# Kernel tuning notes

Hardware: AMD Instinct MI355X
Metric: run time of the kernel (lower is better)

## Reference

```python
import jax, jax.numpy as jnp
import numpy as np

NE, NR = 100000, 200
STT, ABS, REL, RDIM = 512, 256, 256, 384
GAMMA = 12.0
PI = 3.141592653589793
EMB_RNG_R = float(np.sqrt(6.0 / (NR + RDIM)))
B = 8192


def setup_inputs() -> dict:
    key = jax.random.key(0)
    ks = jax.random.split(key, 16)
    cols = [
        jax.random.randint(ks[0], (B, 1), 0, NE),      # s
        jax.random.randint(ks[1], (B, 1), 0, NR),      # r
        jax.random.randint(ks[2], (B, 1), 0, NE),      # o
        jax.random.randint(ks[3], (B, 1), 0, 31),      # d
        jax.random.randint(ks[4], (B, 1), 0, 12),      # m
        jax.random.randint(ks[5], (B, 1), 0, 100),     # y
        jax.random.randint(ks[6], (B, 2 * NR), 0, 1000),  # context times
    ]
    x = jnp.concatenate(cols, axis=1).astype(jnp.int64)
    s = 0.02
    return {
        "x": x,
        "e_emb": jax.random.normal(ks[7], (NE, STT), jnp.float32) * s,
        "r_emb": jax.random.normal(ks[8], (NR, RDIM), jnp.float32) * s,
        "d_frq": jax.random.normal(ks[9], (NE, ABS), jnp.float32) * s,
        "d_phi": jax.random.normal(ks[10], (NE, ABS), jnp.float32) * s,
        "d_amp": jax.random.normal(ks[11], (NE, ABS // 2), jnp.float32) * s,
        "m_frq": jax.random.normal(ks[12], (NE, ABS), jnp.float32) * s,
        "m_phi": jax.random.normal(ks[13], (NE, ABS), jnp.float32) * s,
        "m_amp": jax.random.normal(ks[14], (NE, ABS // 2), jnp.float32) * s,
        "w_e": jax.random.normal(ks[15], (STT, REL // 2), jnp.float32) * s,
        "w_rp": jax.random.normal(jax.random.fold_in(key, 99), (NR, NR, 1), jnp.float32) * s,
    }


def _pos_emb(t):  # t: float [N] -> [N, REL]
    f = 1.0 / (10000.0 ** (jnp.arange(0, REL, 2, dtype=jnp.float32) / REL))
    rs = t[:, None] * f[None, :]
    return jnp.concatenate([jnp.cos(rs), jnp.sin(rs)], axis=1)


def reference(x, e_emb, r_emb, d_frq, d_phi, d_amp, m_frq, m_phi, m_amp, w_e, w_rp):
    f32 = jnp.float32

    def t_emb(e, d, m):  # e int [B], d,m float [B,1] -> [B, ABS]
        re_d, im_d = jnp.split(d * d_frq[e] + d_phi[e], 2, axis=1)
        ad = d_amp[e]
        demb = jnp.concatenate([ad * jnp.cos(re_d), ad * jnp.sin(im_d)], axis=1)
        re_m, im_m = jnp.split(m * m_frq[e] + m_phi[e], 2, axis=1)
        am = m_amp[e]
        memb = jnp.concatenate([am * jnp.cos(re_m), am * jnp.sin(im_m)], axis=1)
        return demb + memb

    def e_p_emb(e):  # e: [B,1,STT] -> [B,1,REL]
        re_w, im_w = jnp.split(w_e, 2, axis=0)
        re_e, im_e = jnp.split(e, 2, axis=2)
        re_p = re_e @ re_w - im_e @ im_w
        im_p = im_e @ re_w - re_e @ im_w  # note: minus, matching source
        return jnp.concatenate([re_p, im_p], axis=2)

    def e_r_emb(r_idx, e_t):  # e_t: [B,NR] float -> [B,REL,1]
        er = _pos_emb(e_t.reshape(-1)).reshape(e_t.shape[0], NR, REL)
        er = jnp.transpose(er, (0, 2, 1))  # [B,REL,NR]
        return jnp.einsum('bdn,bno->bdo', er, w_rp[r_idx])

    s_idx, r_idx, o_idx = x[:, 0], x[:, 1], x[:, 2]
    d_abs = x[:, 3:4].astype(f32)
    m_abs = x[:, 4:5].astype(f32)
    c_s = x[:, -2 * NR:-NR].astype(f32)
    c_o = x[:, -NR:].astype(f32)

    s = e_emb[s_idx][:, None, :]
    s_t = t_emb(s_idx, d_abs, m_abs)[:, None, :]
    s_p = e_p_emb(s)
    s_r = e_r_emb(r_idx, c_s)

    o = e_emb[o_idx][:, None, :]
    o_t = t_emb(o_idx, d_abs, m_abs)[:, None, :]
    o_p = e_p_emb(o)
    o_r = e_r_emb(r_idx, c_o)

    r = r_emb[r_idx][:, None, :]  # [B,1,RDIM]
    p_r = r / (EMB_RNG_R / PI)
    re_r, im_r = jnp.cos(p_r), jnp.sin(p_r)

    re_s, im_s = jnp.split(s, 2, axis=2)
    re_st, im_st = jnp.split(s_t, 2, axis=2)
    re_s = jnp.concatenate([re_s, re_st], axis=2)  # [B,1,RDIM]
    im_s = jnp.concatenate([im_s, im_st], axis=2)
    re_o, im_o = jnp.split(o, 2, axis=2)
    re_ot, im_ot = jnp.split(o_t, 2, axis=2)
    re_o = jnp.concatenate([re_o, re_ot], axis=2)
    im_o = jnp.concatenate([im_o, im_ot], axis=2)

    # RotatE complex rotation score on static+absolute part
    re_sc = re_s * re_r - im_s * im_r - re_o
    im_sc = re_s * im_r + im_s * re_r - im_o
    sc_abs = jnp.sqrt(re_sc * re_sc + im_sc * im_sc).sum(axis=2)

    # relative-time score from projected embeddings + relation-context embeddings
    s_rel = s_p + jnp.transpose(s_r, (0, 2, 1))  # [B,1,REL]
    o_rel = o_p + jnp.transpose(o_r, (0, 2, 1))
    re_sr, im_sr = jnp.split(s_rel, 2, axis=2)
    re_or, im_or = jnp.split(o_rel, 2, axis=2)
    dre, dim = re_sr - re_or, im_sr - im_or
    sc_rel = jnp.sqrt(dre * dre + dim * dim).sum(axis=2)

    return GAMMA - (sc_abs + sc_rel)  # [B,1]
```

## Files before the change

### kernel.cpp

```cpp
#include <hip/hip_runtime.h>
#include <cstdint>

#define B_ROWS 8192
#define XSTR   406
#define GAMMA_C 12.0f
#define SCALE_ANG 30.994217f

#define KH     1024

#define NG_BLK 2048
#define NS_BLK 4096
#define NT_BLK 128
#define NW_BLK 64
#define NPREP  (NG_BLK + NS_BLK + NT_BLK + NW_BLK)

#define TF_BYTES    (KH*256*2)
#define WCAT_BYTES  (512*256*2)
#define G_BYTES     (8192*KH*2)
#define SAB_BYTES   (8192*4)
#define WS_FULL     ((size_t)(TF_BYTES + WCAT_BYTES + G_BYTES + SAB_BYTES))
#define OLDTAB_BYTES (1000*256*2)
#define WS_OLD       ((size_t)(OLDTAB_BYTES + WCAT_BYTES))

typedef __attribute__((ext_vector_type(8))) short short8v;
typedef __attribute__((ext_vector_type(4))) float float4v;

__device__ __forceinline__ float bfLo(uint32_t u) { return __uint_as_float(u << 16); }
__device__ __forceinline__ float bfHi(uint32_t u) { return __uint_as_float(u & 0xffff0000u); }
__device__ __forceinline__ float bf1(unsigned short u) { return __uint_as_float((uint32_t)u << 16); }

__device__ __forceinline__ uint32_t f2bf_u(float x) {
  uint32_t u = __float_as_uint(x);
  u += 0x7fffu + ((u >> 16) & 1u);
  return u >> 16;
}
__device__ __forceinline__ unsigned short f2bf(float x) { return (unsigned short)f2bf_u(x); }

__device__ __forceinline__ short8v cvt8(float4 a, float4 b) {
  short8v r;
  r[0] = (short)f2bf(a.x); r[1] = (short)f2bf(a.y);
  r[2] = (short)f2bf(a.z); r[3] = (short)f2bf(a.w);
  r[4] = (short)f2bf(b.x); r[5] = (short)f2bf(b.y);
  r[6] = (short)f2bf(b.z); r[7] = (short)f2bf(b.w);
  return r;
}

__global__ __launch_bounds__(256) void kge_prep2(
    const int* __restrict__ x, const float* __restrict__ w_rp,
    const float* __restrict__ w_e, const float* __restrict__ e_emb,
    const float* __restrict__ r_emb,
    const float* __restrict__ d_frq, const float* __restrict__ d_phi, const float* __restrict__ d_amp,
    const float* __restrict__ m_frq, const float* __restrict__ m_phi, const float* __restrict__ m_amp,
    unsigned short* __restrict__ tf, unsigned short* __restrict__ wcat,
    unsigned short* __restrict__ G, float* __restrict__ sabs_buf) {
  __shared__ float Hl[4][KH];
  __shared__ float st2[2][2][256];
  __shared__ float redl[4];
  const int bid = blockIdx.x;
  const int tid = threadIdx.x;
  const int sub = tid >> 6, l = tid & 63;

  if (bid < NG_BLK) {
    const int row = bid * 4 + sub;
    float4 z = {0, 0, 0, 0};
    for (int i = l; i < KH / 4; i += 64) ((float4*)Hl[sub])[i] = z;
    const int rid = x[(size_t)row * XSTR + 1];
    const int* cp = x + (size_t)row * XSTR + 6;
    const float* wp = w_rp + (size_t)rid * 200;
    for (int n = l; n < 200; n += 64) {
      float wv = wp[n];
      atomicAdd(&Hl[sub][cp[n]], wv);
      atomicAdd(&Hl[sub][cp[200 + n]], -wv);
    }
    unsigned short* dst = G + (size_t)row * KH;
    for (int i = l; i < KH / 2; i += 64) {
      float a = Hl[sub][2 * i], b = Hl[sub][2 * i + 1];
      ((uint32_t*)dst)[i] = f2bf_u(a) | (f2bf_u(b) << 16);
    }
  } else if (bid < NG_BLK + NS_BLK) {
    const int rsub = tid >> 7;
    const int row = (bid - NG_BLK) * 2 + rsub;
    const int j = tid & 127;
    const int* xr = x + (size_t)row * XSTR;
    const int eS = xr[0], rid = xr[1], eO = xr[2];
    const float dv = (float)xr[3], mv = (float)xr[4];
    const int j2 = 2 * j;
    #pragma unroll
    for (int ent = 0; ent < 2; ++ent) {
      const int e = ent ? eO : eS;
      float2 fd = *(const float2*)&d_frq[(size_t)e * 256 + j2];
      float2 pd = *(const float2*)&d_phi[(size_t)e * 256 + j2];
      float2 fm = *(const float2*)&m_frq[(size_t)e * 256 + j2];
      float2 pm = *(const float2*)&m_phi[(size_t)e * 256 + j2];
      const int ja = j2 & 127;
      float2 ad = *(const float2*)&d_amp[(size_t)e * 128 + ja];
      float2 am = *(const float2*)&m_amp[(size_t)e * 128 + ja];
      float a0 = fmaf(dv, fd.x, pd.x), a1 = fmaf(dv, fd.y, pd.y);
      float b0 = fmaf(mv, fm.x, pm.x), b1 = fmaf(mv, fm.y, pm.y);
      float t0, t1, u0, u1;
      if (j2 < 128) { t0 = __cosf(a0); t1 = __cosf(a1); u0 = __cosf(b0); u1 = __cosf(b1); }
      else          { t0 = __sinf(a0); t1 = __sinf(a1); u0 = __sinf(b0); u1 = __sinf(b1); }
      st2[rsub][ent][j2]     = fmaf(ad.x, t0, am.x * u0);
      st2[rsub][ent][j2 + 1] = fmaf(ad.y, t1, am.y * u1);
    }
    __syncthreads();
    const float* Es = e_emb + (size_t)eS * 512;
    const float* Eo = e_emb + (size_t)eO * 512;
    const float* Rr = r_emb + (size_t)rid * 384;
    float sabs = 0.f;
    #pragma unroll
    for (int t3 = 0; t3 < 3; ++t3) {
      const int u = t3 * 128 + j;
      float ang = Rr[u] * SCALE_ANG;
      float sr = __sinf(ang), cr = __cosf(ang);
      float res, ims, reo, imo;
      if (t3 < 2) {
        res = Es[u]; ims = Es[256 + u];
        reo = Eo[u]; imo = Eo[256 + u];
      } else {
        res = st2[rsub][0][j]; ims = st2[rsub][0][128 + j];
        reo = st2[rsub][1][j]; imo = st2[rsub][1][128 + j];
      }
      float rsc = res * cr - ims * sr - reo;
      float isc = res * sr + ims * cr - imo;
      sabs += sqrtf(rsc * rsc + isc * isc);
    }
    #pragma unroll
    for (int off = 32; off > 0; off >>= 1) sabs += __shfl_down(sabs, off);
    if (l == 0) redl[sub] = sabs;
    __syncthreads();
    if (j == 0) sabs_buf[row] = redl[2 * rsub] + redl[2 * rsub + 1];
  } else if (bid < NG_BLK + NS_BLK + NT_BLK) {
    const int fragid = (bid - NG_BLK - NS_BLK) * 4 + sub;
    const int kt = fragid >> 4, nt = fragid & 15;
    const int c = nt * 16 + (l & 15);
    const float f = exp2f(-(float)(c & 127) * (13.287712379549449f / 128.f));
    __align__(16) unsigned short v[8];
    #pragma unroll
    for (int jj = 0; jj < 8; ++jj) {
      int k = kt * 32 + ((l >> 4) << 3) + jj;
      float val = 0.f;
      if (k < 1000) {
        float s, cv;
        sincosf((float)k * f, &s, &cv);
        val = (c < 128) ? cv : s;
      }
      v[jj] = f2bf(val);
    }
    ((uint4*)tf)[fragid * 64 + l] = *(const uint4*)v;
  } else {
    const int fragid = (bid - NG_BLK - NS_BLK - NT_BLK) * 4 + sub;
    const int kk = fragid >> 4, nt = fragid & 15;
    const int c = nt * 16 + (l & 15);
    __align__(16) unsigned short v[8];
    #pragma unroll
    for (int jj = 0; jj < 8; ++jj) {
      int k = kk * 32 + ((l >> 4) << 3) + jj;
      float s = (k < 256) ? 1.f : -1.f;
      float val = (c < 128) ? s * w_e[k * 128 + c]
                            : -s * w_e[(k ^ 256) * 128 + (c - 128)];
      v[jj] = f2bf(val);
    }
    ((uint4*)wcat)[fragid * 64 + l] = *(const uint4*)v;
  }
}

__global__ __launch_bounds__(256) void kge_fused4(
    const int* __restrict__ x, const float* __restrict__ e_emb,
    const unsigned short* __restrict__ G,
    const unsigned short* __restrict__ wcat, const unsigned short* __restrict__ tf,
    const float* __restrict__ sabs_buf, float* __restrict__ out) {
  __shared__ float part[4][16][256];
  __shared__ float prel[4][16];
  const int tid = threadIdx.x;
  const int w = tid >> 6, l = tid & 63;
  const int m0 = blockIdx.x * 16;

  const int rowA = m0 + (l & 15);
  const int* xrA = x + (size_t)rowA * XSTR;
  const float* Esp = e_emb + (size_t)xrA[0] * 512 + ((l >> 4) << 3);
  const float* Eop = e_emb + (size_t)xrA[2] * 512 + ((l >> 4) << 3);
  const unsigned short* Gp = G + (size_t)rowA * KH + ((l >> 4) << 3);
  const short8v* wq = (const short8v*)wcat;
  const short8v* tq = (const short8v*)tf;

  float4v acc[16];
  #pragma unroll
  for (int i = 0; i < 16; ++i) acc[i] = (float4v){0, 0, 0, 0};

  const int k0 = w * 12;
  #pragma unroll 2
  for (int kt = k0; kt < k0 + 12; ++kt) {
    short8v a;
    const short8v* bsrc;
    if (kt < 16) {
      float4 s0 = *(const float4*)(Esp + kt * 32);
      float4 s1 = *(const float4*)(Esp + kt * 32 + 4);
      float4 o0 = *(const float4*)(Eop + kt * 32);
      float4 o1 = *(const float4*)(Eop + kt * 32 + 4);
      float4 d0 = {s0.x - o0.x, s0.y - o0.y, s0.z - o0.z, s0.w - o0.w};
      float4 d1 = {s1.x - o1.x, s1.y - o1.y, s1.z - o1.z, s1.w - o1.w};
      a = cvt8(d0, d1);
      bsrc = wq + (size_t)kt * 1024;
    } else {
      a = *(const short8v*)(Gp + (kt - 16) * 32);
      bsrc = tq + (size_t)(kt - 16) * 1024;
    }
    #pragma unroll
    for (int nt = 0; nt < 16; ++nt)
      acc[nt] = __builtin_amdgcn_mfma_f32_16x16x32_bf16(a, bsrc[nt * 64 + l], acc[nt], 0, 0, 0);
  }
  #pragma unroll
  for (int nt = 0; nt < 16; ++nt)
    #pragma unroll
    for (int q = 0; q < 4; ++q)
      part[w][nt][q * 64 + l] = acc[nt][q];
  __syncthreads();

  {
    float sq[4] = {0.f, 0.f, 0.f, 0.f};
    #pragma unroll
    for (int pp = 0; pp < 2; ++pp) {
      const int p = 2 * w + pp;
      #pragma unroll
      for (int q = 0; q < 4; ++q) {
        float dre = part[0][p][q * 64 + l] + part[1][p][q * 64 + l]
                  + part[2][p][q * 64 + l] + part[3][p][q * 64 + l];
        float dim = part[0][p + 8][q * 64 + l] + part[1][p + 8][q * 64 + l]
                  + part[2][p + 8][q * 64 + l] + part[3][p + 8][q * 64 + l];
        sq[q] += sqrtf(dre * dre + dim * dim);
      }
    }
    #pragma unroll
    for (int q = 0; q < 4; ++q) {
      float s = sq[q];
      s += __shfl_xor(s, 1); s += __shfl_xor(s, 2);
      s += __shfl_xor(s, 4); s += __shfl_xor(s, 8);
      if ((l & 15) == 0) prel[w][(l >> 4) * 4 + q] = s;
    }
  }
  __syncthreads();
  if (tid < 16) {
    const int r = tid;
    float srel = prel[0][r] + prel[1][r] + prel[2][r] + prel[3][r];
    out[m0 + r] = GAMMA_C - (sabs_buf[m0 + r] + srel);
  }
}

#define NTH    512
#define RPB    8
#define ERB    (2*RPB)
#define APAD   520

__global__ void kge_table_old(unsigned short* __restrict__ tab) {
  int t = blockIdx.x;
  int j = threadIdx.x;
  double f = pow(10000.0, -(double)j / 128.0);
  double ang = (double)t * f;
  int q = j >> 1, lo = j & 1;
  tab[t * 256 + 4 * q + lo]     = f2bf((float)cos(ang));
  tab[t * 256 + 4 * q + 2 + lo] = f2bf((float)sin(ang));
}

__global__ void kge_wcat_old(const float* __restrict__ w_e, unsigned short* __restrict__ wcat) {
  int bid = blockIdx.x;
  int kk = bid >> 4, nt = bid & 15;
  int l = threadIdx.x;
  __align__(16) unsigned short v[8];
  int c = nt * 16 + (l & 15);
  #pragma unroll
  for (int j = 0; j < 8; ++j) {
    int k = kk * 32 + ((l >> 4) << 3) + j;
    float s = (k < 256) ? 1.f : -1.f;
    float val = (c < 128) ? s * w_e[k * 128 + c]
                          : -s * w_e[(k ^ 256) * 128 + (c - 128)];
    v[j] = f2bf(val);
  }
  ((uint4*)wcat)[bid * 64 + l] = *(const uint4*)v;
}

__global__ __launch_bounds__(NTH, 4) void kge_main3(
    const int* __restrict__ x,
    const float* __restrict__ e_emb, const float* __restrict__ r_emb,
    const float* __restrict__ d_frq, const float* __restrict__ d_phi, const float* __restrict__ d_amp,
    const float* __restrict__ m_frq, const float* __restrict__ m_phi, const float* __restrict__ m_amp,
    const float* __restrict__ w_rp,
    const unsigned short* __restrict__ tab, const unsigned short* __restrict__ wcat,
    float* __restrict__ out) {
  __shared__ __align__(16) unsigned short A[ERB][APAD];
  __shared__ __align__(16) unsigned short stb[ERB][256];
  __shared__ __align__(16) float p[ERB][256];
  __shared__ int meta[RPB][6];

  const int tid = threadIdx.x;
  const int base_row = blockIdx.x * RPB;
  const int w = tid >> 6, l = tid & 63;

  if (tid < RPB * 6) {
    int r = tid / 6, f = tid % 6;
    meta[r][f] = x[(size_t)(base_row + r) * XSTR + f];
  }
  __syncthreads();

  for (int i = tid; i < ERB * 128; i += NTH) {
    int er = i >> 7, k4 = i & 127;
    int e = (er & 1) ? meta[er >> 1][2] : meta[er >> 1][0];
    float4 v = ((const float4*)e_emb)[(size_t)e * 128 + k4];
    uint2 pk;
    pk.x = f2bf_u(v.x) | (f2bf_u(v.y) << 16);
    pk.y = f2bf_u(v.z) | (f2bf_u(v.w) << 16);
    *(uint2*)&A[er][k4 * 4] = pk;
  }
  for (int it = tid; it < ERB * 256; it += NTH) {
    int j = it & 255, er = it >> 8, r = er >> 1;
    int e = (er & 1) ? meta[r][2] : meta[r][0];
    float dv = (float)meta[r][3], mv = (float)meta[r][4];
    size_t b256 = (size_t)e * 256 + j, b128 = (size_t)e * 128 + (j & 127);
    float argd = fmaf(dv, d_frq[b256], d_phi[b256]);
    float argm = fmaf(mv, m_frq[b256], m_phi[b256]);
    float vd = (j < 128) ? d_amp[b128] * __cosf(argd) : d_amp[b128] * __sinf(argd);
    float vm = (j < 128) ? m_amp[b128] * __cosf(argm) : m_amp[b128] * __sinf(argm);
    stb[er][j] = f2bf(vd + vm);
  }

  float s0 = 0, s1 = 0, s2 = 0, s3 = 0, o0 = 0, o1 = 0, o2 = 0, o3 = 0;
  {
    const int wu  = __builtin_amdgcn_readfirstlane(w);
    const int rid = __builtin_amdgcn_readfirstlane(meta[wu][1]);
    const int*   cp = x + (size_t)(base_row + wu) * XSTR + 6;
    const float* wp = w_rp + (size_t)rid * 200;
    const uint2* tl = ((const uint2*)tab) + l;
    #pragma unroll 2
    for (int n = 0; n < 200; ++n) {
      float wv = wp[n];
      int cS = cp[n];
      int cO = cp[200 + n];
      uint2 qs = tl[(size_t)cS * 64];
      uint2 qo = tl[(size_t)cO * 64];
      s0 = fmaf(wv, bfLo(qs.x), s0); s1 = fmaf(wv, bfHi(qs.x), s1);
      s2 = fmaf(wv, bfLo(qs.y), s2); s3 = fmaf(wv, bfHi(qs.y), s3);
      o0 = fmaf(wv, bfLo(qo.x), o0); o1 = fmaf(wv, bfHi(qo.x), o1);
      o2 = fmaf(wv, bfLo(qo.y), o2); o3 = fmaf(wv, bfHi(qo.y), o3);
    }
  }
  __syncthreads();

  {
    float4v acc0 = {0, 0, 0, 0}, acc1 = {0, 0, 0, 0};
    const int nt0 = 2 * w, nt1 = 2 * w + 1;
    const short8v* bp = (const short8v*)wcat;
    const unsigned short* arow = &A[l & 15][(l >> 4) << 3];
    #pragma unroll 8
    for (int kk = 0; kk < 16; ++kk) {
      short8v a  = *(const short8v*)(arow + kk * 32);
      short8v b0 = bp[(kk * 16 + nt0) * 64 + l];
      short8v b1 = bp[(kk * 16 + nt1) * 64 + l];
      acc0 = __builtin_amdgcn_mfma_f32_16x16x32_bf16(a, b0, acc0, 0, 0, 0);
      acc1 = __builtin_amdgcn_mfma_f32_16x16x32_bf16(a, b1, acc1, 0, 0, 0);
    }
    int col = l & 15, rbase = (l >> 4) * 4;
    #pragma unroll
    for (int q = 0; q < 4; ++q) {
      p[rbase + q][nt0 * 16 + col] = acc0[q];
      p[rbase + q][nt1 * 16 + col] = acc1[q];
    }
  }
  __syncthreads();

  {
    int es = 2 * w, eo = 2 * w + 1;
    p[es][2 * l] += s0; p[es][2 * l + 1] += s1;
    p[es][128 + 2 * l] += s2; p[es][129 + 2 * l] += s3;
    p[eo][2 * l] += o0; p[eo][2 * l + 1] += o1;
    p[eo][128 + 2 * l] += o2; p[eo][129 + 2 * l] += o3;
  }
  __syncthreads();

  {
    int r = w;
    int rid = meta[r][1];
    float sabs = 0.f;
    #pragma unroll
    for (int u0 = 0; u0 < 384; u0 += 64) {
      int u = u0 + l;
      float ang = r_emb[(size_t)rid * 384 + u] * SCALE_ANG;
      float sr = __sinf(ang), cr = __cosf(ang);
      float res, ims, reo, imo;
      if (u < 256) {
        res = bf1(A[2 * r][u]);       ims = bf1(A[2 * r][256 + u]);
        reo = bf1(A[2 * r + 1][u]);   imo = bf1(A[2 * r + 1][256 + u]);
      } else {
        int uu = u - 256;
        res = bf1(stb[2 * r][uu]);     ims = bf1(stb[2 * r][128 + uu]);
        reo = bf1(stb[2 * r + 1][uu]); imo = bf1(stb[2 * r + 1][128 + uu]);
      }
      float rsc = res * cr - ims * sr - reo;
      float isc = res * sr + ims * cr - imo;
      sabs += sqrtf(rsc * rsc + isc * isc);
    }
    float srel = 0.f;
    #pragma unroll
    for (int u0 = 0; u0 < 128; u0 += 64) {
      int u = u0 + l;
      float dre = p[2 * r][u] - p[2 * r + 1][u];
      float dim = p[2 * r][128 + u] - p[2 * r + 1][128 + u];
      srel += sqrtf(dre * dre + dim * dim);
    }
    float tot = sabs + srel;
    #pragma unroll
    for (int off = 32; off > 0; off >>= 1) tot += __shfl_down(tot, off);
    if (l == 0) out[base_row + r] = GAMMA_C - tot;
  }
}

extern "C" void kernel_launch(void* const* d_in, const int* in_sizes, int n_in,
                              void* d_out, int out_size, void* d_ws, size_t ws_size,
                              hipStream_t stream) {
  (void)in_sizes; (void)n_in; (void)out_size;
  const int*   x     = (const int*)d_in[0];
  const float* e_emb = (const float*)d_in[1];
  const float* r_emb = (const float*)d_in[2];
  const float* d_frq = (const float*)d_in[3];
  const float* d_phi = (const float*)d_in[4];
  const float* d_amp = (const float*)d_in[5];
  const float* m_frq = (const float*)d_in[6];
  const float* m_phi = (const float*)d_in[7];
  const float* m_amp = (const float*)d_in[8];
  const float* w_e   = (const float*)d_in[9];
  const float* w_rp  = (const float*)d_in[10];
  float* out = (float*)d_out;

  if (ws_size >= WS_FULL) {
    char* base = (char*)d_ws;
    unsigned short* tf    = (unsigned short*)base;
    unsigned short* wcat  = (unsigned short*)(base + TF_BYTES);
    unsigned short* G     = (unsigned short*)(base + TF_BYTES + WCAT_BYTES);
    float*          sabsb = (float*)(base + TF_BYTES + WCAT_BYTES + G_BYTES);
    kge_prep2<<<dim3(NPREP), dim3(256), 0, stream>>>(
        x, w_rp, w_e, e_emb, r_emb, d_frq, d_phi, d_amp, m_frq, m_phi, m_amp,
        tf, wcat, G, sabsb);
    kge_fused4<<<dim3(B_ROWS / 16), dim3(256), 0, stream>>>(
        x, e_emb, G, wcat, tf, sabsb, out);
  } else if (ws_size >= WS_OLD) {
    unsigned short* tab  = (unsigned short*)d_ws;
    unsigned short* wcat = (unsigned short*)((char*)d_ws + OLDTAB_BYTES);
    kge_table_old<<<dim3(1000), dim3(128), 0, stream>>>(tab);
    kge_wcat_old<<<dim3(256), dim3(64), 0, stream>>>(w_e, wcat);
    kge_main3<<<dim3(B_ROWS / RPB), dim3(NTH), 0, stream>>>(
        x, e_emb, r_emb, d_frq, d_phi, d_amp, m_frq, m_phi, m_amp, w_rp,
        tab, wcat, out);
  }
}
```

Measured before the change: 66.82 us.

## Build relation-context histogram in LDS inside fused kernel instead of global G

The per-row scatter histogram of relation-context weights is now built with LDS atomics inside the main MFMA kernel rather than in the prep kernel. This removes the 16 MB bf16 G buffer, which was previously written to global memory and read back. The fused kernel now zeroes a padded 16x1028 LDS tile, scatters into it, and feeds the tile to the MFMAs. The same LDS is reused for the partial-sum reduction. This adds barriers and LDS atomic work to the main kernel, and the larger LDS footprint may lower occupancy.

```diff
diff --git a/kernel.cpp b/kernel.cpp
--- a/kernel.cpp
+++ b/kernel.cpp
@@ -7,18 +7,17 @@
 #define SCALE_ANG 30.994217f
 
 #define KH     1024
-
-#define NG_BLK 2048
+#define HPAD   1028
+
 #define NS_BLK 4096
 #define NT_BLK 128
 #define NW_BLK 64
-#define NPREP  (NG_BLK + NS_BLK + NT_BLK + NW_BLK)
+#define NPREP  (NS_BLK + NT_BLK + NW_BLK)
 
 #define TF_BYTES    (KH*256*2)
 #define WCAT_BYTES  (512*256*2)
-#define G_BYTES     (8192*KH*2)
 #define SAB_BYTES   (8192*4)
-#define WS_FULL     ((size_t)(TF_BYTES + WCAT_BYTES + G_BYTES + SAB_BYTES))
+#define WS_FULL     ((size_t)(TF_BYTES + WCAT_BYTES + SAB_BYTES))
 #define OLDTAB_BYTES (1000*256*2)
 #define WS_OLD       ((size_t)(OLDTAB_BYTES + WCAT_BYTES))
 
@@ -45,41 +44,23 @@
   return r;
 }
 
-__global__ __launch_bounds__(256) void kge_prep2(
-    const int* __restrict__ x, const float* __restrict__ w_rp,
+__global__ __launch_bounds__(256) void kge_prep3(
+    const int* __restrict__ x,
     const float* __restrict__ w_e, const float* __restrict__ e_emb,
     const float* __restrict__ r_emb,
     const float* __restrict__ d_frq, const float* __restrict__ d_phi, const float* __restrict__ d_amp,
     const float* __restrict__ m_frq, const float* __restrict__ m_phi, const float* __restrict__ m_amp,
     unsigned short* __restrict__ tf, unsigned short* __restrict__ wcat,
-    unsigned short* __restrict__ G, float* __restrict__ sabs_buf) {
-  __shared__ float Hl[4][KH];
+    float* __restrict__ sabs_buf) {
   __shared__ float st2[2][2][256];
   __shared__ float redl[4];
   const int bid = blockIdx.x;
   const int tid = threadIdx.x;
   const int sub = tid >> 6, l = tid & 63;
 
-  if (bid < NG_BLK) {
-    const int row = bid * 4 + sub;
-    float4 z = {0, 0, 0, 0};
-    for (int i = l; i < KH / 4; i += 64) ((float4*)Hl[sub])[i] = z;
-    const int rid = x[(size_t)row * XSTR + 1];
-    const int* cp = x + (size_t)row * XSTR + 6;
-    const float* wp = w_rp + (size_t)rid * 200;
-    for (int n = l; n < 200; n += 64) {
-      float wv = wp[n];
-      atomicAdd(&Hl[sub][cp[n]], wv);
-      atomicAdd(&Hl[sub][cp[200 + n]], -wv);
-    }
-    unsigned short* dst = G + (size_t)row * KH;
-    for (int i = l; i < KH / 2; i += 64) {
-      float a = Hl[sub][2 * i], b = Hl[sub][2 * i + 1];
-      ((uint32_t*)dst)[i] = f2bf_u(a) | (f2bf_u(b) << 16);
-    }
-  } else if (bid < NG_BLK + NS_BLK) {
+  if (bid < NS_BLK) {
     const int rsub = tid >> 7;
-    const int row = (bid - NG_BLK) * 2 + rsub;
+    const int row = bid * 2 + rsub;
     const int j = tid & 127;
     const int* xr = x + (size_t)row * XSTR;
     const int eS = xr[0], rid = xr[1], eO = xr[2];
@@ -130,8 +111,8 @@
     if (l == 0) redl[sub] = sabs;
     __syncthreads();
     if (j == 0) sabs_buf[row] = redl[2 * rsub] + redl[2 * rsub + 1];
-  } else if (bid < NG_BLK + NS_BLK + NT_BLK) {
-    const int fragid = (bid - NG_BLK - NS_BLK) * 4 + sub;
+  } else if (bid < NS_BLK + NT_BLK) {
+    const int fragid = (bid - NS_BLK) * 4 + sub;
     const int kt = fragid >> 4, nt = fragid & 15;
     const int c = nt * 16 + (l & 15);
     const float f = exp2f(-(float)(c & 127) * (13.287712379549449f / 128.f));
@@ -149,7 +130,7 @@
     }
     ((uint4*)tf)[fragid * 64 + l] = *(const uint4*)v;
   } else {
-    const int fragid = (bid - NG_BLK - NS_BLK - NT_BLK) * 4 + sub;
+    const int fragid = (bid - NS_BLK - NT_BLK) * 4 + sub;
     const int kk = fragid >> 4, nt = fragid & 15;
     const int c = nt * 16 + (l & 15);
     __align__(16) unsigned short v[8];
@@ -165,22 +146,41 @@
   }
 }
 
-__global__ __launch_bounds__(256) void kge_fused4(
+__global__ __launch_bounds__(256) void kge_fused5(
     const int* __restrict__ x, const float* __restrict__ e_emb,
-    const unsigned short* __restrict__ G,
+    const float* __restrict__ w_rp,
     const unsigned short* __restrict__ wcat, const unsigned short* __restrict__ tf,
     const float* __restrict__ sabs_buf, float* __restrict__ out) {
-  __shared__ float part[4][16][256];
+  __shared__ __align__(16) float lds_f[16 * HPAD];
   __shared__ float prel[4][16];
   const int tid = threadIdx.x;
   const int w = tid >> 6, l = tid & 63;
   const int m0 = blockIdx.x * 16;
 
+  #pragma unroll
+  for (int i = tid; i < 16 * HPAD / 4; i += 256)
+    ((float4*)lds_f)[i] = (float4){0, 0, 0, 0};
+  __syncthreads();
+
+  {
+    const int hr = tid >> 4, sub16 = tid & 15;
+    const int row = m0 + hr;
+    const int* xr = x + (size_t)row * XSTR;
+    const int rid = xr[1];
+    const int* cp = xr + 6;
+    const float* wp = w_rp + (size_t)rid * 200;
+    float* hrow = lds_f + hr * HPAD;
+    for (int n = sub16; n < 200; n += 16) {
+      float wv = wp[n];
+      atomicAdd(&hrow[cp[n]], wv);
+      atomicAdd(&hrow[cp[200 + n]], -wv);
+    }
+  }
+
   const int rowA = m0 + (l & 15);
   const int* xrA = x + (size_t)rowA * XSTR;
   const float* Esp = e_emb + (size_t)xrA[0] * 512 + ((l >> 4) << 3);
   const float* Eop = e_emb + (size_t)xrA[2] * 512 + ((l >> 4) << 3);
-  const unsigned short* Gp = G + (size_t)rowA * KH + ((l >> 4) << 3);
   const short8v* wq = (const short8v*)wcat;
   const short8v* tq = (const short8v*)tf;
 
@@ -188,33 +188,43 @@
   #pragma unroll
   for (int i = 0; i < 16; ++i) acc[i] = (float4v){0, 0, 0, 0};
 
-  const int k0 = w * 12;
-  #pragma unroll 2
-  for (int kt = k0; kt < k0 + 12; ++kt) {
-    short8v a;
-    const short8v* bsrc;
-    if (kt < 16) {
-      float4 s0 = *(const float4*)(Esp + kt * 32);
-      float4 s1 = *(const float4*)(Esp + kt * 32 + 4);
-      float4 o0 = *(const float4*)(Eop + kt * 32);
-      float4 o1 = *(const float4*)(Eop + kt * 32 + 4);
-      float4 d0 = {s0.x - o0.x, s0.y - o0.y, s0.z - o0.z, s0.w - o0.w};
-      float4 d1 = {s1.x - o1.x, s1.y - o1.y, s1.z - o1.z, s1.w - o1.w};
-      a = cvt8(d0, d1);
-      bsrc = wq + (size_t)kt * 1024;
-    } else {
-      a = *(const short8v*)(Gp + (kt - 16) * 32);
-      bsrc = tq + (size_t)(kt - 16) * 1024;
-    }
+  #pragma unroll
+  for (int kt = 4 * w; kt < 4 * w + 4; ++kt) {
+    float4 s0 = *(const float4*)(Esp + kt * 32);
+    float4 s1 = *(const float4*)(Esp + kt * 32 + 4);
+    float4 o0 = *(const float4*)(Eop + kt * 32);
+    float4 o1 = *(const float4*)(Eop + kt * 32 + 4);
+    float4 d0 = {s0.x - o0.x, s0.y - o0.y, s0.z - o0.z, s0.w - o0.w};
+    float4 d1 = {s1.x - o1.x, s1.y - o1.y, s1.z - o1.z, s1.w - o1.w};
+    short8v a = cvt8(d0, d1);
+    const short8v* bsrc = wq + (size_t)kt * 1024;
     #pragma unroll
     for (int nt = 0; nt < 16; ++nt)
       acc[nt] = __builtin_amdgcn_mfma_f32_16x16x32_bf16(a, bsrc[nt * 64 + l], acc[nt], 0, 0, 0);
   }
+  __syncthreads();
+
+  {
+    const float* hbase = lds_f + (l & 15) * HPAD + ((l >> 4) << 3);
+    #pragma unroll
+    for (int g = 8 * w; g < 8 * w + 8; ++g) {
+      float4 h0 = *(const float4*)(hbase + g * 32);
+      float4 h1 = *(const float4*)(hbase + g * 32 + 4);
+      short8v a = cvt8(h0, h1);
+      const short8v* bsrc = tq + (size_t)g * 1024;
+      #pragma unroll
+      for (int nt = 0; nt < 16; ++nt)
+        acc[nt] = __builtin_amdgcn_mfma_f32_16x16x32_bf16(a, bsrc[nt * 64 + l], acc[nt], 0, 0, 0);
+    }
+  }
+  __syncthreads();
+
+  float* part = lds_f;
   #pragma unroll
   for (int nt = 0; nt < 16; ++nt)
     #pragma unroll
     for (int q = 0; q < 4; ++q)
-      part[w][nt][q * 64 + l] = acc[nt][q];
+      part[((w * 16 + nt) * 256) + q * 64 + l] = acc[nt][q];
   __syncthreads();
 
   {
@@ -224,10 +234,11 @@
       const int p = 2 * w + pp;
       #pragma unroll
       for (int q = 0; q < 4; ++q) {
-        float dre = part[0][p][q * 64 + l] + part[1][p][q * 64 + l]
-                  + part[2][p][q * 64 + l] + part[3][p][q * 64 + l];
-        float dim = part[0][p + 8][q * 64 + l] + part[1][p + 8][q * 64 + l]
-                  + part[2][p + 8][q * 64 + l] + part[3][p + 8][q * 64 + l];
+        const int idx = q * 64 + l;
+        float dre = part[(0 * 16 + p) * 256 + idx] + part[(1 * 16 + p) * 256 + idx]
+                  + part[(2 * 16 + p) * 256 + idx] + part[(3 * 16 + p) * 256 + idx];
+        float dim = part[(0 * 16 + p + 8) * 256 + idx] + part[(1 * 16 + p + 8) * 256 + idx]
+                  + part[(2 * 16 + p + 8) * 256 + idx] + part[(3 * 16 + p + 8) * 256 + idx];
         sq[q] += sqrtf(dre * dre + dim * dim);
       }
     }
@@ -434,13 +445,12 @@
     char* base = (char*)d_ws;
     unsigned short* tf    = (unsigned short*)base;
     unsigned short* wcat  = (unsigned short*)(base + TF_BYTES);
-    unsigned short* G     = (unsigned short*)(base + TF_BYTES + WCAT_BYTES);
-    float*          sabsb = (float*)(base + TF_BYTES + WCAT_BYTES + G_BYTES);
-    kge_prep2<<<dim3(NPREP), dim3(256), 0, stream>>>(
-        x, w_rp, w_e, e_emb, r_emb, d_frq, d_phi, d_amp, m_frq, m_phi, m_amp,
-        tf, wcat, G, sabsb);
-    kge_fused4<<<dim3(B_ROWS / 16), dim3(256), 0, stream>>>(
-        x, e_emb, G, wcat, tf, sabsb, out);
+    float*          sabsb = (float*)(base + TF_BYTES + WCAT_BYTES);
+    kge_prep3<<<dim3(NPREP), dim3(256), 0, stream>>>(
+        x, w_e, e_emb, r_emb, d_frq, d_phi, d_amp, m_frq, m_phi, m_amp,
+        tf, wcat, sabsb);
+    kge_fused5<<<dim3(B_ROWS / 16), dim3(256), 0, stream>>>(
+        x, e_emb, w_rp, wcat, tf, sabsb, out);
   } else if (ws_size >= WS_OLD) {
     unsigned short* tab  = (unsigned short*)d_ws;
     unsigned short* wcat = (unsigned short*)((char*)d_ws + OLDTAB_BYTES);
```

Result: faster. 59.30 us (median of 2 runs) (-11.3%).
